# Optimization experiments

Measured on AMD Instinct MI355X. Metric: run time of the kernel, lower is better.

The kernel has to match this reference:

```python
import jax, jax.numpy as jnp
import numpy as np

B, S, E, H, V2, L, T = 512, 49, 1024, 1024, 16, 64, 48
D_IN = E + V2 + 1 + L  # LSTM input size = 1105


def setup_inputs() -> dict:
    key = jax.random.key(0)
    ks = jax.random.split(key, 16)
    sd_h = 1.0 / np.sqrt(H)
    u = lambda k, shape, s: jax.random.uniform(k, shape, jnp.float32, -s, s)
    length = jax.random.randint(ks[0], (B,), 1, T + 1).at[0].set(T)
    return {
        'image': jax.random.normal(ks[1], (B, S, E), jnp.float32),
        'view_position': jax.random.uniform(ks[2], (B, V2), jnp.float32),
        'label': jax.random.uniform(ks[3], (B, T + 1, L), jnp.float32),
        'length': length,
        'fc_h_w': u(ks[4], (H, E), 1.0 / np.sqrt(E)),
        'fc_h_b': u(ks[5], (H,), 1.0 / np.sqrt(E)),
        'fc_m_w': u(ks[6], (H, E), 1.0 / np.sqrt(E)),
        'fc_m_b': u(ks[7], (H,), 1.0 / np.sqrt(E)),
        'w_ih': u(ks[8], (4 * H, D_IN), sd_h),
        'w_hh': u(ks[9], (4 * H, H), sd_h),
        'b_ih': u(ks[10], (4 * H,), sd_h),
        'b_hh': u(ks[11], (4 * H,), sd_h),
        'fc_w': u(ks[12], (L + H + 2, H), sd_h),
        'fc_b': u(ks[13], (L + H + 2,), sd_h),
    }


def reference(image, view_position, label, length,
              fc_h_w, fc_h_b, fc_m_w, fc_m_b,
              w_ih, w_hh, b_ih, b_hh, fc_w, fc_b):
    image_mean = image.mean(1)                              # (B, E)
    h0 = jnp.tanh(image_mean @ fc_h_w.T + fc_h_b)           # (B, H)
    m0 = jnp.tanh(image_mean @ fc_m_w.T + fc_m_b)

    # teacher-forced label input: zeros at t=0, then label[:, t-1]
    lab_in = jnp.concatenate([jnp.zeros((B, 1, L), jnp.float32),
                              label[:, :T - 1]], 1)          # (B, T, L)
    lab_in = jnp.transpose(lab_in, (1, 0, 2))                # (T, B, L)
    t_idx = jnp.arange(T)
    begin = (t_idx == 0).astype(jnp.float32)[:, None, None] * jnp.ones((T, B, 1), jnp.float32)
    mask = (t_idx[:, None] < length[None, :]).astype(jnp.float32)[:, :, None]  # (T, B, 1)

    def step(carry, xs):
        h, m = carry
        lab_t, begin_t, mask_t = xs
        x = jnp.concatenate([image_mean, view_position, begin_t, lab_t], 1)  # (B, D_IN)
        gates = x @ w_ih.T + b_ih + h @ w_hh.T + b_hh                        # (B, 4H)
        i, f, g, o = jnp.split(gates, 4, axis=1)
        m_new = jax.nn.sigmoid(f) * m + jax.nn.sigmoid(i) * jnp.tanh(g)
        h_new = jax.nn.sigmoid(o) * jnp.tanh(m_new)
        out = h_new @ fc_w.T + fc_b                                          # (B, L+H+2)
        _lab = jax.nn.sigmoid(out[:, :L]) * mask_t
        _topic = jax.nn.relu(out[:, L:L + H]) * mask_t
        _stop = jax.nn.sigmoid(out[:, L + H:L + H + 1]) * mask_t
        _temp = jnp.exp(out[:, L + H + 1:]) * mask_t
        return (h_new, m_new), (_lab, _topic, _stop, _temp)

    _, (lab_o, topic_o, stop_o, temp_o) = jax.lax.scan(step, (h0, m0), (lab_in, begin, mask))
    # shapes: (T, B, L), (T, B, H), (T, B, 1), (T, B, 1) -- matches pad_sequence layout
    return lab_o, topic_o, stop_o, temp_o
```

## Files before the change

kernel.cpp:

```cpp
#include <hip/hip_runtime.h>
#include <hip/hip_bf16.h>
#include <cstdint>


typedef __bf16 bf16_t;
typedef bf16_t bf16x8 __attribute__((ext_vector_type(8)));
typedef bf16_t bf16x4 __attribute__((ext_vector_type(4)));
typedef float  f32x4  __attribute__((ext_vector_type(4)));

#define Bn    512
#define Sn    49
#define En    1024
#define Hn    1024
#define Ln    64
#define Tn    48
#define DINn  1105
#define NOn   1090
#define HLD   1088
#define HSTEP 557056

#define BM   64
#define LDSP 72

__device__ __forceinline__ float sigm(float x){ return 1.0f / (1.0f + __expf(-x)); }

__global__ __launch_bounds__(256) void k_mean(const float* __restrict__ image,
                                              bf16_t* __restrict__ imb){
  int b  = blockIdx.x;
  int e0 = threadIdx.x * 4;
  const float* p = image + (size_t)b * (Sn * En) + e0;
  float4 acc = make_float4(0.f, 0.f, 0.f, 0.f);
  for (int s = 0; s < Sn; ++s){
    float4 v = *reinterpret_cast<const float4*>(p + (size_t)s * En);
    acc.x += v.x; acc.y += v.y; acc.z += v.z; acc.w += v.w;
  }
  const float inv = 1.0f / 49.0f;
  bf16x4 o;
  o[0] = (bf16_t)(acc.x * inv); o[1] = (bf16_t)(acc.y * inv);
  o[2] = (bf16_t)(acc.z * inv); o[3] = (bf16_t)(acc.w * inv);
  *reinterpret_cast<bf16x4*>(imb + (size_t)b * En + e0) = o;
}

__global__ __launch_bounds__(256) void k_convert(
    const float* __restrict__ w_hh,  const float* __restrict__ fc_h_w,
    const float* __restrict__ fc_m_w,const float* __restrict__ fc_w,
    const float* __restrict__ label, const float* __restrict__ w_ih,
    bf16_t* __restrict__ whht,  bf16_t* __restrict__ fchwb,
    bf16_t* __restrict__ fcmwb, bf16_t* __restrict__ fcwb,
    bf16_t* __restrict__ wimgb, bf16_t* __restrict__ hs){
  const int E0 = 32 * 17 * 16 * 512;
  const int E1 = E0 + 1024 * 1024;
  const int E2 = E1 + 1024 * 1024;
  const int E3 = E2 + 1090 * 1024;
  const int E4 = E3 + 4096 * 1024;
  const int E5 = E4 + 48 * 512 * 64;
  int stride = gridDim.x * blockDim.x;
  for (int i = blockIdx.x * blockDim.x + threadIdx.x; i < E5; i += stride){
    if (i < E0){
      int e = i & 7, l = (i >> 3) & 63, g = (i >> 9) & 15;
      int rest = i >> 13;
      int kt = rest % 17, cbb = rest / 17;
      int wv = g >> 2, ni = (g >> 1) & 1, kk = g & 1;
      int n = wv * 1024 + cbb * 32 + ni * 16 + (l & 15);
      int k = kt * 64 + kk * 32 + (l >> 4) * 8 + e;
      float v = (k < 1024) ? w_hh[(size_t)n * 1024 + k]
                           : w_ih[(size_t)n * DINn + 1041 + (k - 1024)];
      whht[i] = (bf16_t)v;
    } else if (i < E1){ int j = i - E0; fchwb[j] = (bf16_t)fc_h_w[j]; }
    else if (i < E2){ int j = i - E1; fcmwb[j] = (bf16_t)fc_m_w[j]; }
    else if (i < E3){ int j = i - E2; fcwb[j]  = (bf16_t)fc_w[j]; }
    else if (i < E4){
      int j = i - E3; int n = j >> 10, k = j & 1023;
      wimgb[j] = (bf16_t)w_ih[(size_t)n * DINn + k];
    } else {
      int j = i - E4;
      int t = j >> 15, rem = j & 32767, row = rem >> 6, c = rem & 63;
      float v = (t == 0) ? 0.f : label[(size_t)row * (Sn * Ln) + (t - 1) * 64 + c];
      hs[((size_t)t * 512 + row) * HLD + 1024 + c] = (bf16_t)v;
    }
  }
}

__global__ __launch_bounds__(256) void k_vpc(const float* __restrict__ w_ih,
                                             const float* __restrict__ vp,
                                             const float* __restrict__ b_ih,
                                             const float* __restrict__ b_hh,
                                             float* __restrict__ xconst){
  int idx = blockIdx.x * 256 + threadIdx.x;
  int b = idx >> 12, n = idx & 4095;
  float acc = b_ih[n] + b_hh[n];
  const float* w = w_ih + (size_t)n * DINn + En;
  const float* v = vp + b * 16;
  #pragma unroll
  for (int j = 0; j < 16; ++j) acc += v[j] * w[j];
  xconst[idx] = acc;
}

__device__ __forceinline__ void stageAp(bf16_t* sA, const bf16_t* gptr, int ld, int tid){
  #pragma unroll
  for (int i = 0; i < 2; ++i){
    int idx = tid + i * 256;
    int r = idx >> 3, v = idx & 7;
    *reinterpret_cast<bf16x8*>(sA + r * LDSP + v * 8) =
      *reinterpret_cast<const bf16x8*>(gptr + (size_t)r * ld + v * 8);
  }
}

__device__ __forceinline__ void mma_tile(const bf16_t* sA, const bf16_t* sB,
                                         f32x4 (&acc)[4][2], int lane, int w){
  int lr = lane & 15;
  int lk = (lane >> 4) * 8;
  #pragma unroll
  for (int kk = 0; kk < 2; ++kk){
    bf16x8 a[4], bb[2];
    #pragma unroll
    for (int mi = 0; mi < 4; ++mi)
      a[mi] = *reinterpret_cast<const bf16x8*>(sA + (mi * 16 + lr) * LDSP + kk * 32 + lk);
    #pragma unroll
    for (int ni = 0; ni < 2; ++ni)
      bb[ni] = *reinterpret_cast<const bf16x8*>(sB + (w * 32 + ni * 16 + lr) * LDSP + kk * 32 + lk);
    #pragma unroll
    for (int mi = 0; mi < 4; ++mi)
      #pragma unroll
      for (int ni = 0; ni < 2; ++ni)
        acc[mi][ni] = __builtin_amdgcn_mfma_f32_16x16x32_bf16(a[mi], bb[ni], acc[mi][ni], 0, 0, 0);
  }
}

__global__ __launch_bounds__(256) void k_init_gemm(
    const bf16_t* __restrict__ imb,  const bf16_t* __restrict__ fchw,
    const bf16_t* __restrict__ fcmw, const bf16_t* __restrict__ wimg,
    const float* __restrict__ fc_h_b,const float* __restrict__ fc_m_b,
    bf16_t* __restrict__ h0, float* __restrict__ m0, float* __restrict__ xconst){
  __shared__ __align__(16) unsigned char smem[(BM + 128) * LDSP * 2];
  bf16_t* sA = (bf16_t*)smem;
  bf16_t* sB = (bf16_t*)(smem + BM * LDSP * 2);
  int tid = threadIdx.x;
  int cb = blockIdx.x, rb = blockIdx.y;
  int nBase = cb * 128;
  const bf16_t* Bsrc; int nOff;
  if      (nBase < 1024){ Bsrc = fchw; nOff = nBase; }
  else if (nBase < 2048){ Bsrc = fcmw; nOff = nBase - 1024; }
  else                  { Bsrc = wimg; nOff = nBase - 2048; }

  f32x4 acc[4][2] = {};
  int lane = tid & 63, w = tid >> 6;
  for (int kt = 0; kt < 16; ++kt){
    stageAp(sA, imb + (size_t)(rb * 64) * 1024 + kt * 64, 1024, tid);
    #pragma unroll
    for (int i = 0; i < 4; ++i){
      int idx = tid + i * 256;
      int r = idx >> 3, v = idx & 7;
      *reinterpret_cast<bf16x8*>(sB + r * LDSP + v * 8) =
        *reinterpret_cast<const bf16x8*>(Bsrc + (size_t)(nOff + r) * 1024 + kt * 64 + v * 8);
    }
    __syncthreads();
    mma_tile(sA, sB, acc, lane, w);
    __syncthreads();
  }
  int lr = lane & 15, lg = lane >> 4;
  #pragma unroll
  for (int mi = 0; mi < 4; ++mi)
    #pragma unroll
    for (int ni = 0; ni < 2; ++ni)
      #pragma unroll
      for (int r = 0; r < 4; ++r){
        int ng   = nBase + w * 32 + ni * 16 + lr;
        int rowg = rb * 64 + mi * 16 + lg * 4 + r;
        float v = acc[mi][ni][r];
        if (ng < 1024){
          h0[(size_t)rowg * HLD + ng] = (bf16_t)tanhf(v + fc_h_b[ng]);
        } else if (ng < 2048){
          int n = ng - 1024;
          m0[(size_t)rowg * 1024 + n] = tanhf(v + fc_m_b[n]);
        } else {
          int n = ng - 2048;
          xconst[(size_t)rowg * 4096 + n] += v;
        }
      }
}

__global__ __launch_bounds__(256) void k_step(
    const bf16_t* __restrict__ hin,
    bf16_t* __restrict__ hout,
    const bf16_t* __restrict__ whht,
    const float* __restrict__ xconst,
    const float* __restrict__ w_ih,
    float* __restrict__ m,
    int t){
  __shared__ __align__(16) unsigned char smem[40960];
  float* gbuf = (float*)smem;
  int tid = threadIdx.x;
  int cb = blockIdx.x, rb = blockIdx.y;
  int lane = tid & 63, w = tid >> 6;
  int rsub = lane >> 3;
  int usw  = (((lane & 7) ^ rsub) & 7) * 8;
  int lr = lane & 15;
  int key = lr & 7;
  int ub = lane >> 4;
  f32x4 acc[4][2] = {};

  const bf16_t* bbase = whht + (((size_t)cb * 17) << 13) + ((w * 4) << 9) + lane * 8;

  bf16x8 breg[3][2][2];

  auto stageA = [&](int buf, int kt){
    char* base = (char*)smem + buf * 8192;
    #pragma unroll
    for (int c = 0; c < 2; ++c){
      int q = w * 2 + c;
      int r = q * 8 + rsub;
      const bf16_t* g = hin + (size_t)(rb * 64 + r) * HLD + kt * 64 + usw;
      __builtin_amdgcn_global_load_lds((const void*)g, (void*)(base + q * 1024), 16, 0, 0);
    }
  };

  #pragma unroll
  for (int ni = 0; ni < 2; ++ni)
    #pragma unroll
    for (int kk = 0; kk < 2; ++kk){
      breg[0][ni][kk] = *reinterpret_cast<const bf16x8*>(bbase + ((ni * 2 + kk) << 9));
      breg[1][ni][kk] = *reinterpret_cast<const bf16x8*>(bbase + ((size_t)1 << 13) + ((ni * 2 + kk) << 9));
    }
  stageA(0, 0); stageA(1, 1); stageA(2, 2); stageA(3, 3);

  #pragma unroll
  for (int kt = 0; kt < 17; ++kt){
    if (kt + 2 <= 16){
      const int s2 = (kt + 2) % 3;
      #pragma unroll
      for (int ni = 0; ni < 2; ++ni)
        #pragma unroll
        for (int kk = 0; kk < 2; ++kk)
          breg[s2][ni][kk] = *reinterpret_cast<const bf16x8*>(
              bbase + ((size_t)(kt + 2) << 13) + ((ni * 2 + kk) << 9));
    }
    if (kt + 4 <= 16) stageA((kt + 4) % 5, kt + 4);
    asm volatile("s_waitcnt vmcnt(8)" ::: "memory");
    __builtin_amdgcn_sched_barrier(0);
    __builtin_amdgcn_s_barrier();
    const bf16_t* sA = (const bf16_t*)((const char*)smem + (kt % 5) * 8192);
    const int s = kt % 3;
    #pragma unroll
    for (int kk = 0; kk < 2; ++kk){
      int uo = ((kk * 4 + ub) ^ key) * 8;
      bf16x8 a[4];
      #pragma unroll
      for (int mi = 0; mi < 4; ++mi)
        a[mi] = *reinterpret_cast<const bf16x8*>(sA + (mi * 16 + lr) * 64 + uo);
      #pragma unroll
      for (int mi = 0; mi < 4; ++mi){
        acc[mi][0] = __builtin_amdgcn_mfma_f32_16x16x32_bf16(a[mi], breg[s][0][kk], acc[mi][0], 0, 0, 0);
        acc[mi][1] = __builtin_amdgcn_mfma_f32_16x16x32_bf16(a[mi], breg[s][1][kk], acc[mi][1], 0, 0, 0);
      }
    }
    __builtin_amdgcn_s_barrier();
  }
  __syncthreads();

  int lg = lane >> 4;
  #pragma unroll
  for (int mi = 0; mi < 4; ++mi)
    #pragma unroll
    for (int ni = 0; ni < 2; ++ni)
      #pragma unroll
      for (int r = 0; r < 4; ++r){
        int cl = ni * 16 + lr;
        int ng = w * 1024 + cb * 32 + cl;
        int rl = mi * 16 + lg * 4 + r;
        int rowg = rb * 64 + rl;
        float v = acc[mi][ni][r] + xconst[(size_t)rowg * 4096 + ng];
        if (t == 0) v += w_ih[(size_t)ng * DINn + 1040];
        gbuf[(w * 64 + rl) * 33 + cl] = v;
      }
  __syncthreads();
  #pragma unroll
  for (int rep = 0; rep < 8; ++rep){
    int cell = tid + rep * 256;
    int rl = cell >> 5, cl = cell & 31;
    float gi = gbuf[(0 * 64 + rl) * 33 + cl];
    float gf = gbuf[(1 * 64 + rl) * 33 + cl];
    float gg = gbuf[(2 * 64 + rl) * 33 + cl];
    float go = gbuf[(3 * 64 + rl) * 33 + cl];
    int rowg = rb * 64 + rl, colg = cb * 32 + cl;
    size_t o = (size_t)rowg * 1024 + colg;
    float mo = m[o];
    float mn = sigm(gf) * mo + sigm(gi) * tanhf(gg);
    m[o] = mn;
    float hn = sigm(go) * tanhf(mn);
    hout[(size_t)rowg * HLD + colg] = (bf16_t)hn;
  }
}

__global__ __launch_bounds__(256) void k_out(
    const bf16_t* __restrict__ h,
    const bf16_t* __restrict__ fcwb,
    const float* __restrict__ fc_b, const int* __restrict__ length,
    float* __restrict__ out){
  __shared__ __align__(16) unsigned char smem[(BM + 128) * LDSP * 2];
  bf16_t* sA = (bf16_t*)smem;
  bf16_t* sB = (bf16_t*)(smem + BM * LDSP * 2);
  int tid = threadIdx.x;
  int id  = blockIdx.x;
  int xcd = id & 7;
  int rem = id >> 3;
  int cb  = rem % 9;
  int grp = rem / 9;
  int rb  = xcd + 8 * grp;
  f32x4 acc[4][2] = {};
  int lane = tid & 63, w = tid >> 6;
  for (int kt = 0; kt < 16; ++kt){
    stageAp(sA, h + (size_t)(rb * 64) * HLD + kt * 64, HLD, tid);
    #pragma unroll
    for (int i = 0; i < 4; ++i){
      int idx = tid + i * 256;
      int r = idx >> 3, v = idx & 7;
      int n = cb * 128 + r;
      bf16x8 val = {};
      if (n < NOn)
        val = *reinterpret_cast<const bf16x8*>(fcwb + (size_t)n * 1024 + kt * 64 + v * 8);
      *reinterpret_cast<bf16x8*>(sB + r * LDSP + v * 8) = val;
    }
    __syncthreads();
    mma_tile(sA, sB, acc, lane, w);
    __syncthreads();
  }
  int lr = lane & 15, lg = lane >> 4;
  #pragma unroll
  for (int mi = 0; mi < 4; ++mi)
    #pragma unroll
    for (int ni = 0; ni < 2; ++ni)
      #pragma unroll
      for (int r = 0; r < 4; ++r){
        int ng = cb * 128 + w * 32 + ni * 16 + lr;
        if (ng >= NOn) continue;
        int rg = rb * 64 + mi * 16 + lg * 4 + r;
        int tt = rg >> 9, b = rg & 511;
        float v = acc[mi][ni][r] + fc_b[ng];
        float mask = (tt < length[b]) ? 1.0f : 0.0f;
        if      (ng < 64)    out[(size_t)rg * 64 + ng] = sigm(v) * mask;
        else if (ng < 1088)  out[(size_t)1572864 + (size_t)rg * 1024 + (ng - 64)] = fmaxf(v, 0.f) * mask;
        else if (ng == 1088) out[(size_t)26738688 + rg] = sigm(v) * mask;
        else                 out[(size_t)26763264 + rg] = __expf(v) * mask;
      }
}

extern "C" void kernel_launch(void* const* d_in, const int* in_sizes, int n_in,
                              void* d_out, int out_size, void* d_ws, size_t ws_size,
                              hipStream_t stream){
  const float* image  = (const float*)d_in[0];
  const float* vp     = (const float*)d_in[1];
  const float* label  = (const float*)d_in[2];
  const int*   length = (const int*)  d_in[3];
  const float* fc_h_w = (const float*)d_in[4];
  const float* fc_h_b = (const float*)d_in[5];
  const float* fc_m_w = (const float*)d_in[6];
  const float* fc_m_b = (const float*)d_in[7];
  const float* w_ih   = (const float*)d_in[8];
  const float* w_hh   = (const float*)d_in[9];
  const float* b_ih   = (const float*)d_in[10];
  const float* b_hh   = (const float*)d_in[11];
  const float* fc_w   = (const float*)d_in[12];
  const float* fc_b   = (const float*)d_in[13];
  float* out = (float*)d_out;

  char* ws = (char*)d_ws;
  bf16_t* imb    = (bf16_t*)(ws + 0);
  bf16_t* hs     = (bf16_t*)(ws + 1048576);
  float*  m      = (float*) (ws + 55640064);
  float*  xconst = (float*) (ws + 57737216);
  bf16_t* whht   = (bf16_t*)(ws + 66125824);
  bf16_t* wimgb  = (bf16_t*)(ws + 75038720);
  bf16_t* fchwb  = (bf16_t*)(ws + 83427328);
  bf16_t* fcmwb  = (bf16_t*)(ws + 85524480);
  bf16_t* fcwb   = (bf16_t*)(ws + 87621632);

  k_mean   <<<dim3(512),  dim3(256), 0, stream>>>(image, imb);
  k_convert<<<dim3(2048), dim3(256), 0, stream>>>(w_hh, fc_h_w, fc_m_w, fc_w, label, w_ih,
                                                  whht, fchwb, fcmwb, fcwb, wimgb, hs);
  k_vpc    <<<dim3(8192), dim3(256), 0, stream>>>(w_ih, vp, b_ih, b_hh, xconst);
  k_init_gemm<<<dim3(48, 8), dim3(256), 0, stream>>>(imb, fchwb, fcmwb, wimgb,
                                                     fc_h_b, fc_m_b, hs, m, xconst);
  for (int t = 0; t < Tn; ++t){
    k_step<<<dim3(32, 8), dim3(256), 0, stream>>>(hs + (size_t)t * HSTEP,
                                                  hs + (size_t)(t + 1) * HSTEP,
                                                  whht, xconst, w_ih, m, t);
  }
  k_out<<<dim3(3456), dim3(256), 0, stream>>>(hs + (size_t)HSTEP, fcwb, fc_b, length, out);
}
```

Baseline: 912.4 us.

## Rework step and output GEMM pipelines with async LDS loads and deeper prefetch

The recurrent step kernel now uses a uniform 4-slot ring in which the register-held B operand and the LDS-staged A tile advance together, with explicit vmcnt waits and a peeled tail. This replaces the earlier 3-deep B and 5-deep A rings and cuts shared memory use. The output projection kernel moves from synchronous register-to-LDS staging, with a barrier around each k-tile, to a triple-buffered global_load_lds pipeline with swizzled layouts for both operands. The aim is to hide global load latency behind MFMA work, at the cost of more LDS in k_out and hand-tuned wait counts that must exactly match the number of outstanding loads.

```diff
diff --git a/kernel.cpp b/kernel.cpp
--- a/kernel.cpp
+++ b/kernel.cpp
@@ -188,7 +188,7 @@
     const float* __restrict__ w_ih,
     float* __restrict__ m,
     int t){
-  __shared__ __align__(16) unsigned char smem[40960];
+  __shared__ __align__(16) unsigned char smem[33792];
   float* gbuf = (float*)smem;
   int tid = threadIdx.x;
   int cb = blockIdx.x, rb = blockIdx.y;
@@ -201,11 +201,10 @@
   f32x4 acc[4][2] = {};
 
   const bf16_t* bbase = whht + (((size_t)cb * 17) << 13) + ((w * 4) << 9) + lane * 8;
-
-  bf16x8 breg[3][2][2];
-
-  auto stageA = [&](int buf, int kt){
-    char* base = (char*)smem + buf * 8192;
+  bf16x8 breg[4][2][2];
+
+  auto stageA = [&](int slot, int kt){
+    char* base = (char*)smem + slot * 8192;
     #pragma unroll
     for (int c = 0; c < 2; ++c){
       int q = w * 2 + c;
@@ -214,33 +213,17 @@
       __builtin_amdgcn_global_load_lds((const void*)g, (void*)(base + q * 1024), 16, 0, 0);
     }
   };
-
-  #pragma unroll
-  for (int ni = 0; ni < 2; ++ni)
-    #pragma unroll
-    for (int kk = 0; kk < 2; ++kk){
-      breg[0][ni][kk] = *reinterpret_cast<const bf16x8*>(bbase + ((ni * 2 + kk) << 9));
-      breg[1][ni][kk] = *reinterpret_cast<const bf16x8*>(bbase + ((size_t)1 << 13) + ((ni * 2 + kk) << 9));
-    }
-  stageA(0, 0); stageA(1, 1); stageA(2, 2); stageA(3, 3);
-
-  #pragma unroll
-  for (int kt = 0; kt < 17; ++kt){
-    if (kt + 2 <= 16){
-      const int s2 = (kt + 2) % 3;
-      #pragma unroll
-      for (int ni = 0; ni < 2; ++ni)
-        #pragma unroll
-        for (int kk = 0; kk < 2; ++kk)
-          breg[s2][ni][kk] = *reinterpret_cast<const bf16x8*>(
-              bbase + ((size_t)(kt + 2) << 13) + ((ni * 2 + kk) << 9));
-    }
-    if (kt + 4 <= 16) stageA((kt + 4) % 5, kt + 4);
-    asm volatile("s_waitcnt vmcnt(8)" ::: "memory");
-    __builtin_amdgcn_sched_barrier(0);
-    __builtin_amdgcn_s_barrier();
-    const bf16_t* sA = (const bf16_t*)((const char*)smem + (kt % 5) * 8192);
-    const int s = kt % 3;
+  auto loadB = [&](int slot, int kt){
+    #pragma unroll
+    for (int ni = 0; ni < 2; ++ni)
+      #pragma unroll
+      for (int kk = 0; kk < 2; ++kk)
+        breg[slot][ni][kk] = *reinterpret_cast<const bf16x8*>(
+            bbase + ((size_t)kt << 13) + ((ni * 2 + kk) << 9));
+  };
+  auto compute = [&](int kt){
+    const bf16_t* sA = (const bf16_t*)((const char*)smem + (kt & 3) * 8192);
+    const int s = kt & 3;
     #pragma unroll
     for (int kk = 0; kk < 2; ++kk){
       int uo = ((kk * 4 + ub) ^ key) * 8;
@@ -254,8 +237,36 @@
         acc[mi][1] = __builtin_amdgcn_mfma_f32_16x16x32_bf16(a[mi], breg[s][1][kk], acc[mi][1], 0, 0, 0);
       }
     }
+  };
+
+  loadB(0, 0); stageA(0, 0);
+  loadB(1, 1); stageA(1, 1);
+  loadB(2, 2); stageA(2, 2);
+
+  #pragma unroll
+  for (int kt = 0; kt < 14; ++kt){
+    loadB((kt + 3) & 3, kt + 3);
+    stageA((kt + 3) & 3, kt + 3);
+    asm volatile("s_waitcnt vmcnt(18)" ::: "memory");
+    __builtin_amdgcn_sched_barrier(0);
     __builtin_amdgcn_s_barrier();
-  }
+    compute(kt);
+    __builtin_amdgcn_s_barrier();
+  }
+  asm volatile("s_waitcnt vmcnt(12)" ::: "memory");
+  __builtin_amdgcn_sched_barrier(0);
+  __builtin_amdgcn_s_barrier();
+  compute(14);
+  __builtin_amdgcn_s_barrier();
+  asm volatile("s_waitcnt vmcnt(6)" ::: "memory");
+  __builtin_amdgcn_sched_barrier(0);
+  __builtin_amdgcn_s_barrier();
+  compute(15);
+  __builtin_amdgcn_s_barrier();
+  asm volatile("s_waitcnt vmcnt(0)" ::: "memory");
+  __builtin_amdgcn_sched_barrier(0);
+  __builtin_amdgcn_s_barrier();
+  compute(16);
   __syncthreads();
 
   int lg = lane >> 4;
@@ -297,9 +308,7 @@
     const bf16_t* __restrict__ fcwb,
     const float* __restrict__ fc_b, const int* __restrict__ length,
     float* __restrict__ out){
-  __shared__ __align__(16) unsigned char smem[(BM + 128) * LDSP * 2];
-  bf16_t* sA = (bf16_t*)smem;
-  bf16_t* sB = (bf16_t*)(smem + BM * LDSP * 2);
+  __shared__ __align__(16) unsigned char smem[73728];
   int tid = threadIdx.x;
   int id  = blockIdx.x;
   int xcd = id & 7;
@@ -307,25 +316,76 @@
   int cb  = rem % 9;
   int grp = rem / 9;
   int rb  = xcd + 8 * grp;
+  int lane = tid & 63, w = tid >> 6;
+  int rsub = lane >> 3;
+  int usw  = (((lane & 7) ^ rsub) & 7) * 8;
+  int lr = lane & 15;
+  int key = lr & 7;
+  int ub = lane >> 4;
   f32x4 acc[4][2] = {};
-  int lane = tid & 63, w = tid >> 6;
-  for (int kt = 0; kt < 16; ++kt){
-    stageAp(sA, h + (size_t)(rb * 64) * HLD + kt * 64, HLD, tid);
-    #pragma unroll
-    for (int i = 0; i < 4; ++i){
-      int idx = tid + i * 256;
-      int r = idx >> 3, v = idx & 7;
+
+  auto stage = [&](int buf, int kt){
+    char* base = (char*)smem + buf * 24576;
+    #pragma unroll
+    for (int c = 0; c < 2; ++c){
+      int q = w * 2 + c;
+      int r = q * 8 + rsub;
+      const bf16_t* g = h + (size_t)(rb * 64 + r) * HLD + kt * 64 + usw;
+      __builtin_amdgcn_global_load_lds((const void*)g, (void*)(base + q * 1024), 16, 0, 0);
+    }
+    #pragma unroll
+    for (int c = 0; c < 4; ++c){
+      int q = w * 4 + c;
+      int r = q * 8 + rsub;
       int n = cb * 128 + r;
-      bf16x8 val = {};
-      if (n < NOn)
-        val = *reinterpret_cast<const bf16x8*>(fcwb + (size_t)n * 1024 + kt * 64 + v * 8);
-      *reinterpret_cast<bf16x8*>(sB + r * LDSP + v * 8) = val;
-    }
-    __syncthreads();
-    mma_tile(sA, sB, acc, lane, w);
-    __syncthreads();
-  }
-  int lr = lane & 15, lg = lane >> 4;
+      int ncl = (n < NOn) ? n : (NOn - 1);
+      const bf16_t* g = fcwb + (size_t)ncl * 1024 + kt * 64 + usw;
+      __builtin_amdgcn_global_load_lds((const void*)g, (void*)(base + 8192 + q * 1024), 16, 0, 0);
+    }
+  };
+  auto compute = [&](int buf){
+    const bf16_t* sA = (const bf16_t*)((const char*)smem + buf * 24576);
+    const bf16_t* sB = sA + 4096;
+    #pragma unroll
+    for (int kk = 0; kk < 2; ++kk){
+      int uo = ((kk * 4 + ub) ^ key) * 8;
+      bf16x8 a[4], bb[2];
+      #pragma unroll
+      for (int mi = 0; mi < 4; ++mi)
+        a[mi] = *reinterpret_cast<const bf16x8*>(sA + (mi * 16 + lr) * 64 + uo);
+      #pragma unroll
+      for (int ni = 0; ni < 2; ++ni)
+        bb[ni] = *reinterpret_cast<const bf16x8*>(sB + (w * 32 + ni * 16 + lr) * 64 + uo);
+      #pragma unroll
+      for (int mi = 0; mi < 4; ++mi)
+        #pragma unroll
+        for (int ni = 0; ni < 2; ++ni)
+          acc[mi][ni] = __builtin_amdgcn_mfma_f32_16x16x32_bf16(a[mi], bb[ni], acc[mi][ni], 0, 0, 0);
+    }
+  };
+
+  stage(0, 0);
+  stage(1, 1);
+  #pragma unroll
+  for (int kt = 0; kt < 14; ++kt){
+    stage((kt + 2) % 3, kt + 2);
+    asm volatile("s_waitcnt vmcnt(12)" ::: "memory");
+    __builtin_amdgcn_sched_barrier(0);
+    __builtin_amdgcn_s_barrier();
+    compute(kt % 3);
+    __builtin_amdgcn_s_barrier();
+  }
+  asm volatile("s_waitcnt vmcnt(6)" ::: "memory");
+  __builtin_amdgcn_sched_barrier(0);
+  __builtin_amdgcn_s_barrier();
+  compute(14 % 3);
+  __builtin_amdgcn_s_barrier();
+  asm volatile("s_waitcnt vmcnt(0)" ::: "memory");
+  __builtin_amdgcn_sched_barrier(0);
+  __builtin_amdgcn_s_barrier();
+  compute(15 % 3);
+
+  int lg = lane >> 4;
   #pragma unroll
   for (int mi = 0; mi < 4; ++mi)
     #pragma unroll
```

After: 923.0 us. Within noise of the previous version (+1.2%).
